# Kernel tuning notes

Hardware: AMD Instinct MI355X
Metric: run time of the kernel (lower is better)

The kernel has to match this reference:

```python
import jax, jax.numpy as jnp
import numpy as np

BETA = 0.25


def setup_inputs() -> dict:
    key = jax.random.key(0)
    k1, k2, k3, k4 = jax.random.split(key, 4)
    B, D, T, H, W = 2, 256, 8, 32, 32
    K = 8192
    z = jax.random.normal(k1, (B, D, T, H, W), dtype=jnp.float32)
    # nn.init.normal_(embedding.weight, mean=0, std=emb_dim ** -0.5)
    emb_w = jax.random.normal(k2, (K, D), dtype=jnp.float32) * (D ** -0.5)
    # torch Linear default init ~ U(-1/sqrt(in), 1/sqrt(in)); scaled normal is fine for a reference
    w1 = jax.random.normal(k3, (D, D), dtype=jnp.float32) * (D ** -0.5)
    w2 = jax.random.normal(k4, (D, D), dtype=jnp.float32) * (D ** -0.5)
    return {"z": z, "emb_w": emb_w, "w1": w1, "w2": w2}


def reference(z, emb_w, w1, w2):
    B, D, T, H, W = z.shape
    K = emb_w.shape[0]
    # permute to channels-last and flatten: [B,T,H,W,D] -> [N,D]
    z_cl = jnp.transpose(z, (0, 2, 3, 4, 1))
    z_flat = z_cl.reshape(-1, D)
    N = z_flat.shape[0]
    # simvq: Linear -> GELU (exact) -> Linear, both bias-free
    quant_codebook = jax.nn.gelu(emb_w @ w1.T, approximate=False) @ w2.T  # [K, D]
    # pairwise squared L2 distances [N, K]
    d = (
        jnp.sum(z_flat ** 2, axis=1, keepdims=True)
        + jnp.sum(quant_codebook ** 2, axis=1)
        - 2.0 * (z_flat @ quant_codebook.T)
    )
    mean_distance = jnp.mean(d)
    idx = jnp.argmin(d, axis=1)  # [N]
    # gather == one-hot @ codebook
    z_q_flat = quant_codebook[idx]  # [N, D]
    z_q = z_q_flat.reshape(z_cl.shape)
    # VQ loss with stop-gradients
    loss = jnp.mean((jax.lax.stop_gradient(z_q) - z_cl) ** 2) + BETA * jnp.mean(
        (z_q - jax.lax.stop_gradient(z_cl)) ** 2
    )
    # straight-through estimator
    z_q = z_cl + jax.lax.stop_gradient(z_q - z_cl)
    # perplexity from code usage histogram (== mean of one-hot encodings)
    counts = jnp.zeros((K,), dtype=jnp.float32).at[idx].add(1.0)
    e_mean = counts / N
    perplexity = jnp.exp(-jnp.sum(e_mean * jnp.log(e_mean + 1e-10)))
    # back to channels-first [B, D, T, H, W]
    z_q = jnp.transpose(z_q, (0, 4, 1, 2, 3))
    return z_q, loss, perplexity, mean_distance
```

## Files before the change

### kernel.cpp

```cpp
#include <hip/hip_runtime.h>
#include <math.h>

#define BATCH 2
#define DIM   256
#define THW   8192
#define NTOK  16384
#define KCB   8192
#define OUTQ  4194304
#define CAP   2000000
#define SCAP  5600

typedef short short8 __attribute__((ext_vector_type(8)));
typedef float f32x4 __attribute__((ext_vector_type(4)));

__device__ __forceinline__ unsigned short f2bf_rn(float v) {
    unsigned u = __float_as_uint(v);
    unsigned r = u + 0x7FFFu + ((u >> 16) & 1u);
    return (unsigned short)(r >> 16);
}
__device__ __forceinline__ float bf2f(unsigned short b) {
    return __uint_as_float((unsigned)b << 16);
}
__device__ __forceinline__ void gl2lds16(const unsigned short* g, unsigned short* l) {
    __builtin_amdgcn_global_load_lds(
        (const __attribute__((address_space(1))) void*)g,
        (__attribute__((address_space(3))) void*)l, 16, 0, 0);
}

__global__ void k_buildA(const float* __restrict__ z,
                         unsigned short* __restrict__ Ahi,
                         unsigned short* __restrict__ Alo,
                         float* __restrict__ zsq,
                         float* __restrict__ sA, float* __restrict__ sB,
                         float* __restrict__ partialZ) {
    __shared__ ushort2 tile[64][65];
    __shared__ float zacc[64];
    __shared__ float lacc[64];
    __shared__ float pz[256];
    int t = threadIdx.x;
    int n0 = blockIdx.x * 64;
    int b = n0 >> 13;
    int thw0 = n0 & 8191;
    if (t < 64) { zacc[t] = 0.f; lacc[t] = 0.f; }
    pz[t] = 0.f;
    __syncthreads();
    int nn_r = t & 63, dg = t >> 6;
    float a1 = 0.f, a2 = 0.f;
    for (int dc = 0; dc < 256; dc += 64) {
        for (int r = 0; r < 16; ++r) {
            int dd = r * 4 + dg;
            float v = z[((size_t)(b * 256 + dc + dd)) * 8192 + thw0 + nn_r];
            unsigned short hb = f2bf_rn(v);
            float hf = bf2f(hb);
            unsigned short lb = f2bf_rn(v - hf);
            float lf = bf2f(lb);
            tile[dd][nn_r] = make_ushort2(hb, lb);
            a1 += v * v;
            a2 += lf * lf;
        }
        __syncthreads();
        int kk = t & 63, ng = t >> 6;
        float dimsum = 0.f;
        for (int i2 = 0; i2 < 16; ++i2) {
            int nn = ng + i2 * 4;
            ushort2 hl = tile[kk][nn];
            size_t base = (size_t)(n0 + nn) * 256;
            Ahi[base + dc + kk] = hl.x;
            Alo[base + dc + kk] = hl.y;
            dimsum += bf2f(hl.x) + bf2f(hl.y);
        }
        atomicAdd(&pz[dc + kk], dimsum);
        __syncthreads();
    }
    atomicAdd(&zacc[nn_r], a1);
    atomicAdd(&lacc[nn_r], a2);
    __syncthreads();
    if (t < 64) {
        zsq[n0 + t] = zacc[t];
        sA[n0 + t] = 2.1f * sqrtf(lacc[t]);
        sB[n0 + t] = 2.1f * sqrtf(zacc[t]);
    }
    partialZ[blockIdx.x * 256 + t] = pz[t];
}

__global__ void k_splitW(const float* __restrict__ w1, const float* __restrict__ w2,
                         unsigned short* __restrict__ W1s, unsigned short* __restrict__ W2s) {
    int bid = blockIdx.x;
    int row = bid & 255;
    const float* src = (bid >> 8) ? w2 : w1;
    unsigned short* dst = ((bid >> 8) ? W2s : W1s) + (size_t)row * 768;
    int t = threadIdx.x;
    float v = src[row * 256 + t];
    unsigned short hb = f2bf_rn(v);
    unsigned short lb = f2bf_rn(v - bf2f(hb));
    dst[t] = hb;
    dst[256 + t] = hb;
    dst[512 + t] = lb;
}

__global__ void k_buildE(const float* __restrict__ emb, unsigned short* __restrict__ E) {
    int t = threadIdx.x;
    int row = blockIdx.x * 4 + (t >> 6);
    int e4 = (t & 63) * 4;
    float4 v = *(const float4*)&emb[(size_t)row * 256 + e4];
    ushort4 hi, lo;
    hi.x = f2bf_rn(v.x); lo.x = f2bf_rn(v.x - bf2f(hi.x));
    hi.y = f2bf_rn(v.y); lo.y = f2bf_rn(v.y - bf2f(hi.y));
    hi.z = f2bf_rn(v.z); lo.z = f2bf_rn(v.z - bf2f(hi.z));
    hi.w = f2bf_rn(v.w); lo.w = f2bf_rn(v.w - bf2f(hi.w));
    size_t base = (size_t)row * 768;
    *(ushort4*)&E[base + e4] = hi;
    *(ushort4*)&E[base + 256 + e4] = lo;
    *(ushort4*)&E[base + 512 + e4] = hi;
}

template <int GELU>
__global__ __launch_bounds__(256) void k_mlp(const unsigned short* __restrict__ A,
                                             const unsigned short* __restrict__ B,
                                             unsigned short* __restrict__ Hs,
                                             float* __restrict__ C_t) {
    __shared__ __align__(16) char smem[32768];
    unsigned short* Asm = (unsigned short*)smem;
    unsigned short* Bsm = (unsigned short*)(smem + 16384);

    int t = threadIdx.x;
    int lane = t & 63;
    int w = t >> 6;
    int wm = w >> 1, wn = w & 1;
    int m0 = blockIdx.y * 128;
    int n0 = blockIdx.x * 128;

    int rA = w * 8 + (lane >> 3);
    int ch_l = lane & 7;
    int ch_g = ch_l ^ (lane >> 3);
    const unsigned short* gA = A + (size_t)(m0 + rA) * 768 + ch_g * 8;
    const unsigned short* gB = B + (size_t)(n0 + rA) * 768 + ch_g * 8;
    unsigned short* lA = &Asm[rA * 64 + ch_l * 8];
    unsigned short* lB = &Bsm[rA * 64 + ch_l * 8];

    f32x4 acc[4][4];
#pragma unroll
    for (int i = 0; i < 4; ++i)
#pragma unroll
        for (int j = 0; j < 4; ++j)
            acc[i][j] = f32x4{0.f, 0.f, 0.f, 0.f};

#pragma unroll
    for (int i = 0; i < 4; ++i) {
        gl2lds16(gA + (size_t)(32 * i) * 768, lA + 32 * i * 64);
        gl2lds16(gB + (size_t)(32 * i) * 768, lB + 32 * i * 64);
    }
    __syncthreads();

    int l15 = lane & 15;
    int quad = lane >> 4;
    int sw = l15 & 7;
    for (int kc = 0; kc < 12; ++kc) {
#pragma unroll
        for (int kk = 0; kk < 2; ++kk) {
            short8 a[4], b[4];
#pragma unroll
            for (int i = 0; i < 4; ++i)
                a[i] = *(const short8*)&Asm[(wm * 64 + i * 16 + l15) * 64 +
                                            (((kk * 4 + quad) ^ sw) * 8)];
#pragma unroll
            for (int j = 0; j < 4; ++j)
                b[j] = *(const short8*)&Bsm[(wn * 64 + j * 16 + l15) * 64 +
                                            (((kk * 4 + quad) ^ sw) * 8)];
#pragma unroll
            for (int i = 0; i < 4; ++i)
#pragma unroll
                for (int j = 0; j < 4; ++j)
                    acc[i][j] = __builtin_amdgcn_mfma_f32_16x16x32_bf16(a[i], b[j], acc[i][j], 0, 0, 0);
        }
        __syncthreads();
        if (kc < 11) {
            int ko = (kc + 1) * 64;
#pragma unroll
            for (int i = 0; i < 4; ++i) {
                gl2lds16(gA + (size_t)(32 * i) * 768 + ko, lA + 32 * i * 64);
                gl2lds16(gB + (size_t)(32 * i) * 768 + ko, lB + 32 * i * 64);
            }
            __syncthreads();
        }
    }

#pragma unroll
    for (int i = 0; i < 4; ++i) {
#pragma unroll
        for (int reg = 0; reg < 4; ++reg) {
            int mrow = m0 + wm * 64 + i * 16 + quad * 4 + reg;
#pragma unroll
            for (int j = 0; j < 4; ++j) {
                int ncol = n0 + wn * 64 + j * 16 + l15;
                float h = acc[i][j][reg];
                if (GELU) {
                    float g = 0.5f * h * (1.f + erff(h * 0.70710678118654752f));
                    unsigned short hb = f2bf_rn(g);
                    unsigned short lb = f2bf_rn(g - bf2f(hb));
                    size_t base = (size_t)mrow * 768;
                    Hs[base + ncol] = hb;
                    Hs[base + 256 + ncol] = lb;
                    Hs[base + 512 + ncol] = hb;
                } else {
                    C_t[(size_t)mrow * 8192 + ncol] = h;
                }
            }
        }
    }
}

__global__ void k_buildB(const float* __restrict__ C_t,
                         unsigned short* __restrict__ Bhi,
                         unsigned short* __restrict__ Blo,
                         float* __restrict__ csq,
                         float* __restrict__ sC, float* __restrict__ sCl,
                         unsigned* __restrict__ tileMaxC, unsigned* __restrict__ tileMaxCl,
                         float* __restrict__ accums, float* __restrict__ partialC) {
    __shared__ ushort2 tile[64][65];
    __shared__ float kacc[64];
    __shared__ float lacc[64];
    __shared__ float pc[256];
    int t = threadIdx.x;
    int k0 = blockIdx.x * 64;
    if (t < 64) { kacc[t] = 0.f; lacc[t] = 0.f; }
    pc[t] = 0.f;
    __syncthreads();
    int nn_r = t & 63, dg = t >> 6;
    float a1 = 0.f, a2 = 0.f;
    for (int dc = 0; dc < 256; dc += 64) {
        for (int r = 0; r < 16; ++r) {
            int dd = r * 4 + dg;
            float v = C_t[(size_t)(dc + dd) * KCB + k0 + nn_r];
            unsigned short hb = f2bf_rn(v);
            float hf = bf2f(hb);
            unsigned short lb = f2bf_rn(v - hf);
            float lf = bf2f(lb);
            tile[dd][nn_r] = make_ushort2(hb, lb);
            a1 += v * v;
            a2 += lf * lf;
        }
        __syncthreads();
        int kk = t & 63, ng = t >> 6;
        float dimsum = 0.f;
        for (int i2 = 0; i2 < 16; ++i2) {
            int nn = ng + i2 * 4;
            ushort2 hl = tile[kk][nn];
            size_t base = (size_t)(k0 + nn) * 256;
            Bhi[base + dc + kk] = hl.x;
            Blo[base + dc + kk] = hl.y;
            dimsum += bf2f(hl.x) + bf2f(hl.y);
        }
        atomicAdd(&pc[dc + kk], dimsum);
        __syncthreads();
    }
    atomicAdd(&kacc[nn_r], a1);
    atomicAdd(&lacc[nn_r], a2);
    __syncthreads();
    if (t < 64) {
        float c2 = kacc[t], l2 = lacc[t];
        float sc = sqrtf(c2), sl = sqrtf(l2);
        csq[k0 + t] = c2;
        sC[k0 + t] = sc;
        sCl[k0 + t] = sl;
        int tl = blockIdx.x >> 1;
        atomicMax(&tileMaxC[tl], __float_as_uint(sc));
        atomicMax(&tileMaxCl[tl], __float_as_uint(sl));
        atomicMax((unsigned*)&accums[3], __float_as_uint(c2));
        atomicMax((unsigned*)&accums[4], __float_as_uint(l2));
    }
    partialC[blockIdx.x * 256 + t] = pc[t];
}

__global__ __launch_bounds__(512, 2) void k_dist_hi(const unsigned short* __restrict__ A,
                                                    const unsigned short* __restrict__ B,
                                                    const float* __restrict__ zsq,
                                                    const float* __restrict__ csq,
                                                    const float* __restrict__ sA,
                                                    const float* __restrict__ sB,
                                                    const unsigned* __restrict__ tileMaxC,
                                                    const unsigned* __restrict__ tileMaxCl,
                                                    unsigned long long* __restrict__ packed,
                                                    float* __restrict__ accums,
                                                    unsigned long long* __restrict__ cand) {
    __shared__ __align__(16) char smem[131072];
    float* sbd     = (float*)smem;
    float* gprev_s = (float*)(smem + 2048);
    float* thr     = (float*)(smem + 3072);
    unsigned* scnt  = (unsigned*)(smem + 4096);
    unsigned* sbase = (unsigned*)(smem + 4100);
    unsigned long long* scand = (unsigned long long*)(smem + 4112);

    int t = threadIdx.x;
    int lane = t & 63;
    int w = t >> 6;
    int wm = w >> 1, wn = w & 1;

    unsigned f = blockIdx.x + (blockIdx.y << 6);
    unsigned xcd = f & 7, i5 = f >> 3;
    unsigned mb = (xcd & 3) * 16 + (i5 & 15);
    unsigned nb = (xcd >> 2) * 16 + (i5 >> 4);
    int m0 = (int)mb * 256;
    int n0 = (int)nb * 256;

    int rA0 = w * 8 + (lane >> 3);
    int ch_l = lane & 7;
    int ch_g = ch_l ^ (lane >> 3);
    const unsigned short* gA = A + (size_t)(m0 + rA0) * 256 + ch_g * 8;
    const unsigned short* gB = B + (size_t)(n0 + rA0) * 256 + ch_g * 8;
    unsigned short* smemU = (unsigned short*)smem;
    unsigned short* lA = smemU + rA0 * 64 + ch_l * 8;
    unsigned short* lB = smemU + 16384 + rA0 * 64 + ch_l * 8;

    int l15 = lane & 15;
    int quad = lane >> 4;
    int sw = l15 & 7;

    float M1 = sqrtf(accums[3]);
    float M2 = sqrtf(accums[4]);
    float msC  = fmaxf(__uint_as_float(tileMaxC[2 * nb]),
                       __uint_as_float(tileMaxC[2 * nb + 1]));
    float msCl = fmaxf(__uint_as_float(tileMaxCl[2 * nb]),
                       __uint_as_float(tileMaxCl[2 * nb + 1]));

    f32x4 acc[4][8];
#pragma unroll
    for (int i = 0; i < 4; ++i)
#pragma unroll
        for (int j = 0; j < 8; ++j)
            acc[i][j] = f32x4{0.f, 0.f, 0.f, 0.f};

#define STAGE(B_, KO)                                                       \
    {                                                                       \
        int off_ = (B_) * 32768;                                            \
        _Pragma("unroll")                                                   \
        for (int i_ = 0; i_ < 4; ++i_)                                      \
            gl2lds16(gA + (size_t)(64 * i_) * 256 + (KO),                   \
                     lA + off_ + 64 * i_ * 64);                             \
        _Pragma("unroll")                                                   \
        for (int i_ = 0; i_ < 4; ++i_)                                      \
            gl2lds16(gB + (size_t)(64 * i_) * 256 + (KO),                   \
                     lB + off_ + 64 * i_ * 64);                             \
    }

#define KSTEP(KC, BUF, WN, DOSTAGE)                                         \
    {                                                                       \
        __builtin_amdgcn_sched_barrier(0);                                  \
        __builtin_amdgcn_s_barrier();   \
        __builtin_amdgcn_sched_barrier(0);                                  \
        if (DOSTAGE) STAGE((BUF) ^ 1, ((KC) + 1) * 64);                     \
        asm volatile("s_waitcnt vmcnt(" #WN ")" ::: "memory");              \
        __builtin_amdgcn_sched_barrier(0);                                  \
        __builtin_amdgcn_s_barrier();            \
        __builtin_amdgcn_sched_barrier(0);                                  \
        const unsigned short* Ar = smemU + (BUF) * 32768;                   \
        const unsigned short* Br = Ar + 16384;                              \
        _Pragma("unroll")                                                   \
        for (int kk = 0; kk < 2; ++kk) {                                    \
            short8 a[4], b[8];                                              \
            _Pragma("unroll")                                               \
            for (int i = 0; i < 4; ++i)                                     \
                a[i] = *(const short8*)&Ar[(wm * 64 + i * 16 + l15) * 64 +  \
                                           (((kk * 4 + quad) ^ sw) * 8)];   \
            _Pragma("unroll")                                               \
            for (int j = 0; j < 8; ++j)                                     \
                b[j] = *(const short8*)&Br[(wn * 128 + j * 16 + l15) * 64 + \
                                           (((kk * 4 + quad) ^ sw) * 8)];   \
            __builtin_amdgcn_s_setprio(1);                                  \
            _Pragma("unroll")                                               \
            for (int i = 0; i < 4; ++i)                                     \
                _Pragma("unroll")                                           \
                for (int j = 0; j < 8; ++j)                                 \
                    acc[i][j] = __builtin_amdgcn_mfma_f32_16x16x32_bf16(    \
                        a[i], b[j], acc[i][j], 0, 0, 0);                    \
            __builtin_amdgcn_s_setprio(0);                                  \
        }                                                                   \
    }

    STAGE(0, 0)
    KSTEP(0, 0, 8, 1)
    KSTEP(1, 1, 8, 1)
    KSTEP(2, 0, 8, 1)
    KSTEP(3, 1, 0, 0)
#undef KSTEP
#undef STAGE
    __syncthreads();

    float cv[8];
    int cols[8];
#pragma unroll
    for (int j = 0; j < 8; ++j) {
        int cloc = wn * 128 + j * 16 + l15;
        cols[j] = n0 + cloc;
        cv[j] = csq[cols[j]];
    }

    if (t == 0) *scnt = 0;
    if (t < 256) {
        const unsigned* hp = (const unsigned*)&packed[m0 + t];
        gprev_s[t] = __uint_as_float(__atomic_load_n(hp + 1, __ATOMIC_RELAXED));
    }
#pragma unroll
    for (int i = 0; i < 4; ++i) {
#pragma unroll
        for (int reg = 0; reg < 4; ++reg) {
            int rloc = wm * 64 + i * 16 + quad * 4 + reg;
            float zs = zsq[m0 + rloc];
            float bd = 3.4e38f;
#pragma unroll
            for (int j = 0; j < 8; ++j) {
                float d = (zs + cv[j]) - 2.0f * acc[i][j][reg];
                acc[i][j][reg] = d;
                bd = fminf(bd, d);
            }
#pragma unroll
            for (int off = 1; off < 16; off <<= 1)
                bd = fminf(bd, __shfl_xor(bd, off, 64));
            if (l15 == 0) sbd[wn * 256 + rloc] = bd;
        }
    }
    __syncthreads();
    if (t < 256) {
        float bd = fminf(sbd[t], sbd[256 + t]);
        atomicMin(&packed[m0 + t], (unsigned long long)__float_as_uint(bd) << 32);
        float g = fminf(bd, gprev_s[t]);
        thr[t] = g + 1e-3f + sA[m0 + t] * (M1 + msC) + sB[m0 + t] * (M2 + msCl);
    }
    __syncthreads();
    unsigned* cnt = (unsigned*)&accums[2];
#pragma unroll
    for (int i = 0; i < 4; ++i) {
#pragma unroll
        for (int reg = 0; reg < 4; ++reg) {
            int rloc = wm * 64 + i * 16 + quad * 4 + reg;
            float tr = thr[rloc];
            bool p[8];
            bool any = false;
#pragma unroll
            for (int j = 0; j < 8; ++j) {
                p[j] = acc[i][j][reg] <= tr;
                any |= p[j];
            }
            if (__ballot(any)) {
                unsigned rbits = (unsigned)((m0 + rloc) << 13);
#pragma unroll
                for (int j = 0; j < 8; ++j) {
                    if (p[j]) {
                        unsigned long long entry =
                            ((unsigned long long)__float_as_uint(acc[i][j][reg]) << 32) |
                            (rbits | (unsigned)cols[j]);
                        unsigned pos = atomicAdd(scnt, 1u);
                        if (pos < SCAP) scand[pos] = entry;
                        else {
                            unsigned gp2 = atomicAdd(cnt, 1u);
                            if (gp2 < CAP) cand[gp2] = entry;
                        }
                    }
                }
            }
        }
    }
    __syncthreads();
    if (t == 0) {
        unsigned m = *scnt;
        if (m > SCAP) m = SCAP;
        *scnt = m;
        *sbase = atomicAdd(cnt, m);
    }
    __syncthreads();
    {
        unsigned m = *scnt, b0 = *sbase;
        for (unsigned u = t; u < m; u += 512)
            if (b0 + u < CAP) cand[b0 + u] = scand[u];
    }
}

__global__ __launch_bounds__(256) void k_rescore(const unsigned long long* __restrict__ cand,
                                                 const unsigned short* __restrict__ Ahi,
                                                 const unsigned short* __restrict__ Alo,
                                                 const unsigned short* __restrict__ Bhi,
                                                 const unsigned short* __restrict__ Blo,
                                                 const float* __restrict__ zsq,
                                                 const float* __restrict__ csq,
                                                 const float* __restrict__ sA,
                                                 const float* __restrict__ sB,
                                                 const float* __restrict__ sC,
                                                 const float* __restrict__ sCl,
                                                 const unsigned long long* __restrict__ packed,
                                                 unsigned long long* __restrict__ packed2,
                                                 const float* __restrict__ accums) {
    unsigned total = *(const unsigned*)&accums[2];
    if (total > CAP) total = CAP;
    float M1 = sqrtf(accums[3]);
    float M2 = sqrtf(accums[4]);
    int lane = threadIdx.x & 63;
    unsigned wv = blockIdx.x * 4 + (threadIdx.x >> 6);
    unsigned nw = gridDim.x * 4;
    for (unsigned e = wv; e < total; e += nw) {
        unsigned long long ent = cand[e];
        float dhi = __uint_as_float((unsigned)(ent >> 32));
        unsigned nk = (unsigned)ent;
        int n = (nk >> 13) & 16383;
        int k = nk & 8191;
        float g = __uint_as_float((unsigned)(packed[n] >> 32));
        float marg = g + 1e-3f + sA[n] * (M1 + sC[k]) + sB[n] * (M2 + sCl[k]);
        if (dhi > marg) continue;
        ushort4 zh = *((const ushort4*)(Ahi + (size_t)n * 256) + lane);
        ushort4 zl = *((const ushort4*)(Alo + (size_t)n * 256) + lane);
        ushort4 ch = *((const ushort4*)(Bhi + (size_t)k * 256) + lane);
        ushort4 cl = *((const ushort4*)(Blo + (size_t)k * 256) + lane);
        float s = (bf2f(zh.x) + bf2f(zl.x)) * (bf2f(ch.x) + bf2f(cl.x))
                + (bf2f(zh.y) + bf2f(zl.y)) * (bf2f(ch.y) + bf2f(cl.y))
                + (bf2f(zh.z) + bf2f(zl.z)) * (bf2f(ch.z) + bf2f(cl.z))
                + (bf2f(zh.w) + bf2f(zl.w)) * (bf2f(ch.w) + bf2f(cl.w));
#pragma unroll
        for (int off = 1; off < 64; off <<= 1)
            s += __shfl_xor(s, off, 64);
        if (lane == 0) {
            float dd = (zsq[n] + csq[k]) - 2.0f * s;
            unsigned long long p =
                ((unsigned long long)__float_as_uint(dd) << 32) | (unsigned)k;
            atomicMin(&packed2[n], p);
        }
    }
}

__global__ void k_unpack(const unsigned long long* __restrict__ packed2,
                         int* __restrict__ idx, int* __restrict__ counts) {
    int n = blockIdx.x * 256 + threadIdx.x;
    unsigned long long p = packed2[n];
    int k = (int)(p & 0xffffffffull);
    idx[n] = k;
    atomicAdd(&counts[k], 1);
}

__global__ void k_zqloss(const float* __restrict__ z, const float* __restrict__ C_t,
                         const int* __restrict__ idx, float* __restrict__ out,
                         float* __restrict__ loss_sum) {
    __shared__ float red[256];
    int bid = blockIdx.x;
    int b = bid >> 8;
    int d = bid & 255;
    int t = threadIdx.x;
    const float* crow = C_t + (size_t)d * KCB;
    const int* ib = idx + b * THW;
    size_t base = ((size_t)(b * DIM + d)) * THW;
    float lsum = 0.f;
    for (int it = 0; it < 32; ++it) {
        int thw = it * 256 + t;
        int id = ib[thw];
        float v = crow[id];
        float zz = z[base + thw];
        out[base + thw] = v;
        float df = v - zz;
        lsum += df * df;
    }
    red[t] = lsum;
    __syncthreads();
    for (int s = 128; s > 0; s >>= 1) {
        if (t < s) red[t] += red[t + s];
        __syncthreads();
    }
    if (t == 0) atomicAdd(loss_sum, red[0]);
}

__global__ void k_scalars(const int* __restrict__ counts,
                          const float* __restrict__ accums,
                          const float* __restrict__ zsq, const float* __restrict__ csq,
                          const float* __restrict__ partialZ,
                          const float* __restrict__ partialC,
                          float* __restrict__ out_tail) {
    __shared__ double redd[256];
    __shared__ float redf[256];
    int t = threadIdx.x;
    double szsq = 0.0, scsq = 0.0;
    for (int n = t; n < NTOK; n += 256) szsq += (double)zsq[n];
    for (int k = t; k < KCB; k += 256) scsq += (double)csq[k];
    float SZ = 0.f, SC = 0.f;
    for (int b2 = 0; b2 < 256; ++b2) SZ += partialZ[b2 * 256 + t];
    for (int b2 = 0; b2 < 128; ++b2) SC += partialC[b2 * 256 + t];
    double total = 8192.0 * szsq + 16384.0 * scsq - 2.0 * (double)SZ * (double)SC;
    redd[t] = total;
    float s = 0.f;
    for (int k = t; k < KCB; k += 256) {
        float e = (float)counts[k] * (1.0f / 16384.0f);
        s += e * logf(e + 1e-10f);
    }
    redf[t] = s;
    __syncthreads();
    for (int st = 128; st > 0; st >>= 1) {
        if (t < st) { redd[t] += redd[t + st]; redf[t] += redf[t + st]; }
        __syncthreads();
    }
    if (t == 0) {
        out_tail[0] = 1.25f * accums[1] / 4194304.0f;
        out_tail[1] = expf(-redf[0]);
        out_tail[2] = (float)(redd[0] / (16384.0 * 8192.0));
    }
}

extern "C" void kernel_launch(void* const* d_in, const int* in_sizes, int n_in,
                              void* d_out, int out_size, void* d_ws, size_t ws_size,
                              hipStream_t stream) {
    const float* z     = (const float*)d_in[0];
    const float* emb_w = (const float*)d_in[1];
    const float* w1    = (const float*)d_in[2];
    const float* w2    = (const float*)d_in[3];
    float* out = (float*)d_out;

    char* w = (char*)d_ws;
    unsigned short* Ahi = (unsigned short*)(w + 0);
    unsigned short* Alo = (unsigned short*)(w + 8388608);
    unsigned short* Ebf = (unsigned short*)(w + 16777216);
    unsigned short* Bhi = (unsigned short*)(w + 29360128);
    unsigned short* Blo = (unsigned short*)(w + 33554432);
    unsigned short* W1s = (unsigned short*)(w + 37748736);
    unsigned short* W2s = (unsigned short*)(w + 38141952);
    float* zsq   = (float*)(w + 38535168);
    float* sA    = (float*)(w + 38666240);
    float* sB    = (float*)(w + 38731776);
    float* csq   = (float*)(w + 38797312);
    float* sC    = (float*)(w + 38862848);
    float* sCl   = (float*)(w + 38895616);
    unsigned long long* packed  = (unsigned long long*)(w + 38928384);
    unsigned long long* packed2 = (unsigned long long*)(w + 39059456);
    int*   idx    = (int*)(w + 39190528);
    int*   counts = (int*)(w + 39256064);
    float* partialZ = (float*)(w + 39288832);
    float* partialC = (float*)(w + 39550976);
    unsigned* tileMaxC  = (unsigned*)(w + 39682048);
    unsigned* tileMaxCl = (unsigned*)(w + 39682304);
    float* accums = (float*)(w + 39682560);

    float* C_t = (float*)Ebf;
    unsigned short* Hs = (unsigned short*)d_out;
    unsigned long long* cand = (unsigned long long*)d_out;

    hipMemsetAsync(counts, 0, 32768, stream);
    hipMemsetAsync(tileMaxC, 0, 1024, stream);
    hipMemsetAsync(packed, 0xFF, 262144, stream);

    k_buildA<<<NTOK / 64, 256, 0, stream>>>(z, Ahi, Alo, zsq, sA, sB, partialZ);
    k_splitW<<<512, 256, 0, stream>>>(w1, w2, W1s, W2s);
    k_buildE<<<KCB / 4, 256, 0, stream>>>(emb_w, Ebf);

    k_mlp<1><<<dim3(2, KCB / 128), 256, 0, stream>>>(Ebf, W1s, Hs, nullptr);
    k_mlp<0><<<dim3(KCB / 128, 2), 256, 0, stream>>>(W2s, Hs, nullptr, C_t);

    k_buildB<<<KCB / 64, 256, 0, stream>>>(C_t, Bhi, Blo, csq, sC, sCl,
                                           tileMaxC, tileMaxCl, accums, partialC);

    k_dist_hi<<<dim3(NTOK / 256, KCB / 256), 512, 0, stream>>>(
        Ahi, Bhi, zsq, csq, sA, sB, tileMaxC, tileMaxCl, packed, accums, cand);

    k_rescore<<<1024, 256, 0, stream>>>(cand, Ahi, Alo, Bhi, Blo, zsq, csq,
                                        sA, sB, sC, sCl, packed, packed2, accums);

    k_unpack<<<NTOK / 256, 256, 0, stream>>>(packed2, idx, counts);
    k_zqloss<<<BATCH * DIM, 256, 0, stream>>>(z, C_t, idx, out, accums + 1);
    k_scalars<<<1, 256, 0, stream>>>(counts, accums, zsq, csq, partialZ, partialC, out + OUTQ);
}
```

Measured before the change: 401.6 us.

## Reshape distance GEMM warp tiling to 2x4 and interleave staged loads with MFMA phases

Changes the k_dist_hi wave layout from 4x2 (64x128 per wave) to 2x4 (128x64 per wave) and splits each K-chunk into four phases. Each phase reads a slice of A fragments, issues one quarter of the next chunk's global-to-LDS loads, and runs a slice of MFMAs. The goal is finer-grained overlap of memory staging with matrix math and smaller live fragment register sets. The cost is more barriers per K-step, and the shared-memory scratch offsets are shifted to fit the four per-column-group min slots.

```diff
diff --git a/kernel.cpp b/kernel.cpp
--- a/kernel.cpp
+++ b/kernel.cpp
@@ -285,16 +285,16 @@
                                                     unsigned long long* __restrict__ cand) {
     __shared__ __align__(16) char smem[131072];
     float* sbd     = (float*)smem;
-    float* gprev_s = (float*)(smem + 2048);
-    float* thr     = (float*)(smem + 3072);
-    unsigned* scnt  = (unsigned*)(smem + 4096);
-    unsigned* sbase = (unsigned*)(smem + 4100);
-    unsigned long long* scand = (unsigned long long*)(smem + 4112);
+    float* gprev_s = (float*)(smem + 4096);
+    float* thr     = (float*)(smem + 5120);
+    unsigned* scnt  = (unsigned*)(smem + 6144);
+    unsigned* sbase = (unsigned*)(smem + 6148);
+    unsigned long long* scand = (unsigned long long*)(smem + 6160);
 
     int t = threadIdx.x;
     int lane = t & 63;
     int w = t >> 6;
-    int wm = w >> 1, wn = w & 1;
+    int wm = w >> 2, wn = w & 3;
 
     unsigned f = blockIdx.x + (blockIdx.y << 6);
     unsigned xcd = f & 7, i5 = f >> 3;
@@ -303,14 +303,13 @@
     int m0 = (int)mb * 256;
     int n0 = (int)nb * 256;
 
-    int rA0 = w * 8 + (lane >> 3);
-    int ch_l = lane & 7;
-    int ch_g = ch_l ^ (lane >> 3);
-    const unsigned short* gA = A + (size_t)(m0 + rA0) * 256 + ch_g * 8;
-    const unsigned short* gB = B + (size_t)(n0 + rA0) * 256 + ch_g * 8;
+    int rr = t >> 3;
+    int ch_l = t & 7;
+    int ch_g = ch_l ^ (rr & 7);
+    const unsigned short* gA = A + (size_t)(m0 + rr) * 256 + ch_g * 8;
+    const unsigned short* gB = B + (size_t)(n0 + rr) * 256 + ch_g * 8;
     unsigned short* smemU = (unsigned short*)smem;
-    unsigned short* lA = smemU + rA0 * 64 + ch_l * 8;
-    unsigned short* lB = smemU + 16384 + rA0 * 64 + ch_l * 8;
+    int ldsoff = rr * 64 + ch_l * 8;
 
     int l15 = lane & 15;
     int quad = lane >> 4;
@@ -323,74 +322,109 @@
     float msCl = fmaxf(__uint_as_float(tileMaxCl[2 * nb]),
                        __uint_as_float(tileMaxCl[2 * nb + 1]));
 
-    f32x4 acc[4][8];
-#pragma unroll
-    for (int i = 0; i < 4; ++i)
-#pragma unroll
-        for (int j = 0; j < 8; ++j)
+    f32x4 acc[8][4];
+#pragma unroll
+    for (int i = 0; i < 8; ++i)
+#pragma unroll
+        for (int j = 0; j < 4; ++j)
             acc[i][j] = f32x4{0.f, 0.f, 0.f, 0.f};
 
-#define STAGE(B_, KO)                                                       \
+    short8 a[2][2];
+    short8 b[2][4];
+
+#define STAGE_U(TT, Q)                                                      \
     {                                                                       \
-        int off_ = (B_) * 32768;                                            \
+        unsigned short* bb_ = smemU + ((TT) & 1) * 32768 +                  \
+                              (((Q) >= 2) ? 16384 : 0) + ((Q) & 1) * 8192;  \
+        const unsigned short* gg_ = (((Q) < 2) ? gA : gB) +                 \
+                              (size_t)(((Q) & 1) * 128) * 256 + (TT) * 64;  \
+        gl2lds16(gg_, bb_ + ldsoff);                                        \
+        gl2lds16(gg_ + (size_t)64 * 256, bb_ + 4096 + ldsoff);              \
+    }
+
+#define RD_B(TT)                                                            \
+    {                                                                       \
+        const unsigned short* Bb_ = smemU + ((TT) & 1) * 32768 + 16384;     \
         _Pragma("unroll")                                                   \
-        for (int i_ = 0; i_ < 4; ++i_)                                      \
-            gl2lds16(gA + (size_t)(64 * i_) * 256 + (KO),                   \
-                     lA + off_ + 64 * i_ * 64);                             \
+        for (int kk = 0; kk < 2; ++kk)                                      \
+            _Pragma("unroll")                                               \
+            for (int j = 0; j < 4; ++j)                                     \
+                b[kk][j] = *(const short8*)&Bb_[(wn * 64 + j * 16 + l15) *  \
+                            64 + (((kk * 4 + quad) ^ sw) * 8)];             \
+    }
+
+#define RD_A(TT, Q)                                                         \
+    {                                                                       \
+        const unsigned short* Ab_ = smemU + ((TT) & 1) * 32768;             \
         _Pragma("unroll")                                                   \
-        for (int i_ = 0; i_ < 4; ++i_)                                      \
-            gl2lds16(gB + (size_t)(64 * i_) * 256 + (KO),                   \
-                     lB + off_ + 64 * i_ * 64);                             \
-    }
-
-#define KSTEP(KC, BUF, WN, DOSTAGE)                                         \
+        for (int kk = 0; kk < 2; ++kk)                                      \
+            _Pragma("unroll")                                               \
+            for (int ii = 0; ii < 2; ++ii)                                  \
+                a[kk][ii] = *(const short8*)&Ab_[(wm * 128 +                \
+                            (2 * (Q) + ii) * 16 + l15) * 64 +               \
+                            (((kk * 4 + quad) ^ sw) * 8)];                  \
+    }
+
+#define MM(Q)                                                               \
+    __builtin_amdgcn_s_setprio(1);                                          \
+    _Pragma("unroll")                                                       \
+    for (int kk = 0; kk < 2; ++kk)                                          \
+        _Pragma("unroll")                                                   \
+        for (int ii = 0; ii < 2; ++ii)                                      \
+            _Pragma("unroll")                                               \
+            for (int j = 0; j < 4; ++j)                                     \
+                acc[2 * (Q) + ii][j] = __builtin_amdgcn_mfma_f32_16x16x32_bf16( \
+                    a[kk][ii], b[kk][j], acc[2 * (Q) + ii][j], 0, 0, 0);    \
+    __builtin_amdgcn_s_setprio(0);
+
+#define PH0(TT, WNS)                                                        \
     {                                                                       \
-        __builtin_amdgcn_sched_barrier(0);                                  \
-        __builtin_amdgcn_s_barrier();   \
-        __builtin_amdgcn_sched_barrier(0);                                  \
-        if (DOSTAGE) STAGE((BUF) ^ 1, ((KC) + 1) * 64);                     \
-        asm volatile("s_waitcnt vmcnt(" #WN ")" ::: "memory");              \
-        __builtin_amdgcn_sched_barrier(0);                                  \
-        __builtin_amdgcn_s_barrier();            \
-        __builtin_amdgcn_sched_barrier(0);                                  \
-        const unsigned short* Ar = smemU + (BUF) * 32768;                   \
-        const unsigned short* Br = Ar + 16384;                              \
-        _Pragma("unroll")                                                   \
-        for (int kk = 0; kk < 2; ++kk) {                                    \
-            short8 a[4], b[8];                                              \
-            _Pragma("unroll")                                               \
-            for (int i = 0; i < 4; ++i)                                     \
-                a[i] = *(const short8*)&Ar[(wm * 64 + i * 16 + l15) * 64 +  \
-                                           (((kk * 4 + quad) ^ sw) * 8)];   \
-            _Pragma("unroll")                                               \
-            for (int j = 0; j < 8; ++j)                                     \
-                b[j] = *(const short8*)&Br[(wn * 128 + j * 16 + l15) * 64 + \
-                                           (((kk * 4 + quad) ^ sw) * 8)];   \
-            __builtin_amdgcn_s_setprio(1);                                  \
-            _Pragma("unroll")                                               \
-            for (int i = 0; i < 4; ++i)                                     \
-                _Pragma("unroll")                                           \
-                for (int j = 0; j < 8; ++j)                                 \
-                    acc[i][j] = __builtin_amdgcn_mfma_f32_16x16x32_bf16(    \
-                        a[i], b[j], acc[i][j], 0, 0, 0);                    \
-            __builtin_amdgcn_s_setprio(0);                                  \
-        }                                                                   \
-    }
-
-    STAGE(0, 0)
-    KSTEP(0, 0, 8, 1)
-    KSTEP(1, 1, 8, 1)
-    KSTEP(2, 0, 8, 1)
-    KSTEP(3, 1, 0, 0)
-#undef KSTEP
-#undef STAGE
-    __syncthreads();
-
-    float cv[8];
-    int cols[8];
-#pragma unroll
-    for (int j = 0; j < 8; ++j) {
-        int cloc = wn * 128 + j * 16 + l15;
+        if ((TT) < 3) STAGE_U((TT) + 1, 0)                                  \
+        asm volatile("s_waitcnt vmcnt(" WNS ")" ::: "memory");              \
+        __builtin_amdgcn_sched_barrier(0);                                  \
+        __builtin_amdgcn_s_barrier();                                       \
+        __builtin_amdgcn_sched_barrier(0);                                  \
+        RD_B(TT)                                                            \
+        RD_A(TT, 0)                                                         \
+        MM(0)                                                               \
+        __builtin_amdgcn_sched_barrier(0);                                  \
+        __builtin_amdgcn_s_barrier();                                       \
+        __builtin_amdgcn_sched_barrier(0);                                  \
+    }
+
+#define PHQ(TT, Q)                                                          \
+    {                                                                       \
+        RD_A(TT, Q)                                                         \
+        if ((TT) < 3) STAGE_U((TT) + 1, Q)                                  \
+        __builtin_amdgcn_sched_barrier(0);                                  \
+        __builtin_amdgcn_s_barrier();                                       \
+        __builtin_amdgcn_sched_barrier(0);                                  \
+        MM(Q)                                                               \
+        __builtin_amdgcn_sched_barrier(0);                                  \
+        __builtin_amdgcn_s_barrier();                                       \
+        __builtin_amdgcn_sched_barrier(0);                                  \
+    }
+
+    STAGE_U(0, 0) STAGE_U(0, 1) STAGE_U(0, 2) STAGE_U(0, 3)
+
+    PH0(0, "2") PHQ(0, 1) PHQ(0, 2) PHQ(0, 3)
+    PH0(1, "2") PHQ(1, 1) PHQ(1, 2) PHQ(1, 3)
+    PH0(2, "2") PHQ(2, 1) PHQ(2, 2) PHQ(2, 3)
+    PH0(3, "0") PHQ(3, 1) PHQ(3, 2) PHQ(3, 3)
+
+#undef PH0
+#undef PHQ
+#undef MM
+#undef RD_A
+#undef RD_B
+#undef STAGE_U
+    __syncthreads();
+
+    float cv[4];
+    int cols[4];
+#pragma unroll
+    for (int j = 0; j < 4; ++j) {
+        int cloc = wn * 64 + j * 16 + l15;
         cols[j] = n0 + cloc;
         cv[j] = csq[cols[j]];
     }
@@ -401,14 +435,14 @@
         gprev_s[t] = __uint_as_float(__atomic_load_n(hp + 1, __ATOMIC_RELAXED));
     }
 #pragma unroll
-    for (int i = 0; i < 4; ++i) {
+    for (int i = 0; i < 8; ++i) {
 #pragma unroll
         for (int reg = 0; reg < 4; ++reg) {
-            int rloc = wm * 64 + i * 16 + quad * 4 + reg;
+            int rloc = wm * 128 + i * 16 + quad * 4 + reg;
             float zs = zsq[m0 + rloc];
             float bd = 3.4e38f;
 #pragma unroll
-            for (int j = 0; j < 8; ++j) {
+            for (int j = 0; j < 4; ++j) {
                 float d = (zs + cv[j]) - 2.0f * acc[i][j][reg];
                 acc[i][j][reg] = d;
                 bd = fminf(bd, d);
@@ -421,7 +455,8 @@
     }
     __syncthreads();
     if (t < 256) {
-        float bd = fminf(sbd[t], sbd[256 + t]);
+        float bd = fminf(fminf(sbd[t], sbd[256 + t]),
+                         fminf(sbd[512 + t], sbd[768 + t]));
         atomicMin(&packed[m0 + t], (unsigned long long)__float_as_uint(bd) << 32);
         float g = fminf(bd, gprev_s[t]);
         thr[t] = g + 1e-3f + sA[m0 + t] * (M1 + msC) + sB[m0 + t] * (M2 + msCl);
@@ -429,22 +464,22 @@
     __syncthreads();
     unsigned* cnt = (unsigned*)&accums[2];
 #pragma unroll
-    for (int i = 0; i < 4; ++i) {
+    for (int i = 0; i < 8; ++i) {
 #pragma unroll
         for (int reg = 0; reg < 4; ++reg) {
-            int rloc = wm * 64 + i * 16 + quad * 4 + reg;
+            int rloc = wm * 128 + i * 16 + quad * 4 + reg;
             float tr = thr[rloc];
-            bool p[8];
+            bool p[4];
             bool any = false;
 #pragma unroll
-            for (int j = 0; j < 8; ++j) {
+            for (int j = 0; j < 4; ++j) {
                 p[j] = acc[i][j][reg] <= tr;
                 any |= p[j];
             }
             if (__ballot(any)) {
                 unsigned rbits = (unsigned)((m0 + rloc) << 13);
 #pragma unroll
-                for (int j = 0; j < 8; ++j) {
+                for (int j = 0; j < 4; ++j) {
                     if (p[j]) {
                         unsigned long long entry =
                             ((unsigned long long)__float_as_uint(acc[i][j][reg]) << 32) |
```

Result: slower. 421.0 us (+4.8%).
